# Performance work log

Measured on AMD Instinct MI355X. Metric: run time of the kernel, lower is better.

The kernel has to match this reference:

```python
import jax, jax.numpy as jnp
import numpy as np

# Search geometry (matches init_kwargs)
WS, WT, PS, K, STRIDE0 = 9, 1, 7, 10, 4
SEARCH_INPUT = "noisy"
ALPHA = 0.5
CRIT = "l2"


def _extract_patches(vid, ti, hi, wi):
    """vid: [T,H,W,C]; ti/hi/wi int32 with shape [...] (patch top-left corners).
    Returns [..., PS*PS*C] with clamped (edge-replicated) boundary handling."""
    T, H, W, C = vid.shape
    dy = jnp.arange(PS)
    dx = jnp.arange(PS)
    hh = jnp.clip(hi[..., None, None] + dy[:, None], 0, H - 1)  # [...,PS,1]
    ww = jnp.clip(wi[..., None, None] + dx[None, :], 0, W - 1)  # [...,1,PS]
    p = vid[ti[..., None, None], hh, ww]  # [...,PS,PS,C]
    return p.reshape(p.shape[:-3] + (PS * PS * C,))


def _nls(vid, fflow, bflow):
    """NonLocalSearch: vid [T,H,W,C], flows [T,H,W,2] (channel 0 = x/w, 1 = y/h).
    Returns (topk_dists [nq,K], inds = (ti,hi,wi,tk,hk,wk))."""
    T, H, W, C = vid.shape
    nH, nW = H // STRIDE0, W // STRIDE0
    ti, hi, wi = jnp.meshgrid(jnp.arange(T), jnp.arange(nH) * STRIDE0,
                              jnp.arange(nW) * STRIDE0, indexing="ij")
    ti, hi, wi = ti.reshape(-1), hi.reshape(-1), wi.reshape(-1)  # [nq]
    q = _extract_patches(vid, ti, hi, wi)  # [nq, PS*PS*C]

    ff = fflow[ti, hi, wi]  # [nq,2] flow to frame t+1
    bf = bflow[ti, hi, wi]  # [nq,2] flow to frame t-1
    zero = jnp.zeros_like(ff)
    flow_dt = jnp.stack([bf, zero, ff], axis=1)  # [nq, 2*WT+1, 2] for dt=-1,0,+1
    dts = jnp.arange(-WT, WT + 1)
    tj = jnp.clip(ti[:, None] + dts[None, :], 0, T - 1)  # [nq, 2*WT+1]
    bh = jnp.clip(hi[:, None] + jnp.round(flow_dt[..., 1]).astype(jnp.int32), 0, H - 1)
    bw = jnp.clip(wi[:, None] + jnp.round(flow_dt[..., 0]).astype(jnp.int32), 0, W - 1)

    # Candidate schedule: (dt_index, oy, ox) for all (2*WT+1)*WS*WS candidates.
    r = WS // 2
    oy, ox = np.meshgrid(np.arange(-r, r + 1), np.arange(-r, r + 1), indexing="ij")
    nt = 2 * WT + 1
    specs = np.stack([np.repeat(np.arange(nt), WS * WS),
                      np.tile(oy.ravel(), nt),
                      np.tile(ox.ravel(), nt)], axis=1).astype(np.int32)  # [S,3]

    def step(_, spec):
        di, sy, sx = spec[0], spec[1], spec[2]
        tjc = tj[:, di]
        hj = jnp.clip(bh[:, di] + sy, 0, H - 1)
        wj = jnp.clip(bw[:, di] + sx, 0, W - 1)
        cp = _extract_patches(vid, tjc, hj, wj)  # [nq,D]
        d = jnp.sum((q - cp) ** 2, axis=-1)  # L2 patch distance, [nq]
        return None, (d, tjc, hj, wj)

    _, (dists, tjs, hjs, wjs) = jax.lax.scan(step, None, jnp.asarray(specs))
    # dists: [S, nq] -> top-K smallest per query
    negd, idx = jax.lax.top_k(-dists.T, K)  # [nq,K]
    tk = jnp.take_along_axis(tjs.T, idx, axis=1)
    hk = jnp.take_along_axis(hjs.T, idx, axis=1)
    wk = jnp.take_along_axis(wjs.T, idx, axis=1)
    return -negd, (ti, hi, wi, tk, hk, wk)


def _refine(vid, inds):
    """RefineSearch with wr=1,kr=1: recompute L2 patch distances at given inds."""
    ti, hi, wi, tk, hk, wk = inds
    q = _extract_patches(vid, ti, hi, wi)          # [nq, D]
    cp = _extract_patches(vid, tk, hk, wk)         # [nq, K, D]
    return jnp.sum((q[:, None, :] - cp) ** 2, axis=-1)  # [nq, K]


def setup_inputs() -> dict:
    key = jax.random.key(0)
    k1, k2, k3, k4 = jax.random.split(key, 4)
    B, T, C, H, W = 1, 5, 3, 384, 384
    noisy = jax.random.normal(k1, (B, T, C, H, W), dtype=jnp.float32)
    deno = jax.random.normal(k2, (B, T, C, H, W), dtype=jnp.float32)
    fflow = jax.random.normal(k3, (B, T, 2, H, W), dtype=jnp.float32)
    bflow = jax.random.normal(k4, (B, T, 2, H, W), dtype=jnp.float32)
    return {"noisy": noisy, "deno": deno, "fflow": fflow, "bflow": bflow}


def reference(noisy, deno, fflow, bflow):
    def per_video(nv, dv, ff, bf):
        nv_t = jnp.transpose(nv, (0, 2, 3, 1))  # [T,H,W,C]
        dv_t = jnp.transpose(dv, (0, 2, 3, 1))
        ff_t = jnp.transpose(ff, (0, 2, 3, 1))  # [T,H,W,2]
        bf_t = jnp.transpose(bf, (0, 2, 3, 1))
        if SEARCH_INPUT == "noisy":
            srch = nv_t
        elif SEARCH_INPUT == "deno":
            srch = dv_t
        else:  # interp
            srch = ALPHA * nv_t + (1.0 - ALPHA) * dv_t
        _, inds = _nls(srch, ff_t, bf_t)
        return _refine(nv_t, inds)  # [nq, K]

    dists = jax.vmap(per_video)(noisy, deno, fflow, bflow)  # [B, nq, K]
    if CRIT == "l1":
        return jnp.mean(jnp.sqrt(dists))
    return jnp.mean(dists)
```

## Files before the change

### kernel.cpp

```cpp
#include <hip/hip_runtime.h>

#define TT 5
#define HH 384
#define WW 384
#define CC 3
#define WSR 4
#define NH_ 96
#define NW_ 96
#define NQ_ (TT*NH_*NW_)
#define NCAND 243
#define KK 10

#define RROW 12
#define RSST 13

typedef _Float16 h2v __attribute__((ext_vector_type(2)));
union U32H2 { unsigned u; h2v h; };

static __device__ __forceinline__ unsigned pack_f16(float a, float b) {
    U32H2 u;
    u.h.x = (_Float16)a; u.h.y = (_Float16)b;
    return u.u;
}

static __device__ __forceinline__ unsigned wave_min63(unsigned x) {
    x = min(x, (unsigned)__builtin_amdgcn_update_dpp((int)x,(int)x,0x121,0xF,0xF,false));
    x = min(x, (unsigned)__builtin_amdgcn_update_dpp((int)x,(int)x,0x122,0xF,0xF,false));
    x = min(x, (unsigned)__builtin_amdgcn_update_dpp((int)x,(int)x,0x124,0xF,0xF,false));
    x = min(x, (unsigned)__builtin_amdgcn_update_dpp((int)x,(int)x,0x128,0xF,0xF,false));
    x = min(x, (unsigned)__builtin_amdgcn_update_dpp((int)x,(int)x,0x142,0xF,0xF,false));
    x = min(x, (unsigned)__builtin_amdgcn_update_dpp((int)x,(int)x,0x143,0xF,0xF,false));
    return x;
}

__global__ __launch_bounds__(256) void nls_kernel(
    const float* __restrict__ vid,
    const float* __restrict__ fflow,
    const float* __restrict__ bflow,
    float* __restrict__ ws)
{
    const int q   = blockIdx.x;
    const int tid = threadIdx.x;
    const int t   = q / (NH_*NW_);
    const int rem = q % (NH_*NW_);
    const int hi  = (rem / NW_) * 4;
    const int wi  = (rem % NW_) * 4;

    __shared__ alignas(16) unsigned reg_lds[135*RROW];
    __shared__ alignas(16) unsigned qp_lds[84];
    __shared__ alignas(16) float    rssd[189*RSST];
    __shared__ float dist[256];

    const float ffx = fflow[((t*2+0)*HH + hi)*WW + wi];
    const float ffy = fflow[((t*2+1)*HH + hi)*WW + wi];
    const float bfx = bflow[((t*2+0)*HH + hi)*WW + wi];
    const float bfy = bflow[((t*2+1)*HH + hi)*WW + wi];

    const int tj0 = max(t-1, 0);
    const int tj2 = min(t+1, TT-1);
    const int bh0 = min(max(hi + (int)rintf(bfy), 0), HH-1);
    const int bw0 = min(max(wi + (int)rintf(bfx), 0), WW-1);
    const int bh2 = min(max(hi + (int)rintf(ffy), 0), HH-1);
    const int bw2 = min(max(wi + (int)rintf(ffx), 0), WW-1);
    const int rm0 = max(bh0-WSR,0), rm1 = max(hi-WSR,0), rm2 = max(bh2-WSR,0);
    const int cm0 = max(bw0-WSR,0), cm1 = max(wi-WSR,0), cm2 = max(bw2-WSR,0);
    const int ca0 = cm0 & ~1,       ca1 = cm1 & ~1,      ca2 = cm2 & ~1;

    for (int i = tid; i < 270; i += 256) {
        int row = i >> 1, h = i & 1;
        int di  = row / 45; int r45 = row - di*45;
        int c   = r45 / 15; int r   = r45 - c*15;
        int tjd = (di==0)?tj0:((di==1)?t  :tj2);
        int rm  = (di==0)?rm0:((di==1)?rm1:rm2);
        int ca  = (di==0)?ca0:((di==1)?ca1:ca2);
        int rr  = min(rm + r, HH-1);
        const float* vrow = vid + (size_t)((tjd*CC+c)*HH + rr)*WW;
        int c0 = ca + 8*h;
        float f0,f1,f2,f3,f4,f5,f6,f7;
        if (ca <= 368) {
            float2 p0 = *(const float2*)(vrow + c0);
            float2 p1 = *(const float2*)(vrow + c0 + 2);
            float2 p2 = *(const float2*)(vrow + c0 + 4);
            float2 p3 = *(const float2*)(vrow + c0 + 6);
            f0=p0.x; f1=p0.y; f2=p1.x; f3=p1.y; f4=p2.x; f5=p2.y; f6=p3.x; f7=p3.y;
        } else {
            f0=vrow[min(c0,  WW-1)]; f1=vrow[min(c0+1,WW-1)];
            f2=vrow[min(c0+2,WW-1)]; f3=vrow[min(c0+3,WW-1)];
            f4=vrow[min(c0+4,WW-1)]; f5=vrow[min(c0+5,WW-1)];
            f6=vrow[min(c0+6,WW-1)]; f7=vrow[min(c0+7,WW-1)];
        }
        uint4 w;
        w.x = pack_f16(f0,f1); w.y = pack_f16(f2,f3);
        w.z = pack_f16(f4,f5); w.w = pack_f16(f6,f7);
        *(uint4*)&reg_lds[row*RROW + 4*h] = w;
    }
    if (tid < 84) {
        int c  = tid / 28;
        int rr = tid - c*28;
        int dy = rr >> 2;
        int k  = rr & 3;
        int row = min(hi+dy, HH-1);
        const float* vrow = vid + (size_t)((t*CC + c)*HH + row)*WW;
        float v0 = vrow[min(wi + 2*k, WW-1)];
        float v1 = (k==3) ? 0.0f : vrow[min(wi + 2*k + 1, WW-1)];
        qp_lds[tid] = pack_f16(v0, v1);
    }
    __syncthreads();

    if (tid < 189) {
        int di   = tid / 63; int r63 = tid - di*63;
        int roff = r63 / 7;  int dy  = r63 - roff*7;
        int rr   = roff + dy;
        float rs[10];
        #pragma unroll
        for (int w = 0; w < 10; w++) rs[w] = 0.f;
        #pragma unroll
        for (int c = 0; c < 3; c++) {
            int base = ((di*3 + c)*15 + rr)*RROW;
            uint4 va0 = *(const uint4*)&reg_lds[base];
            uint4 va1 = *(const uint4*)&reg_lds[base + 4];
            uint4 vq  = *(const uint4*)&qp_lds[c*28 + dy*4];
            unsigned A[8], B[8];
            A[0]=va0.x; A[1]=va0.y; A[2]=va0.z; A[3]=va0.w;
            A[4]=va1.x; A[5]=va1.y; A[6]=va1.z; A[7]=va1.w;
            #pragma unroll
            for (int j = 0; j < 7; j++) B[j] = (A[j] >> 16) | (A[j+1] << 16);
            B[7] = A[7] >> 16;
            U32H2 q0,q1,q2,q3;
            q0.u = vq.x; q1.u = vq.y; q2.u = vq.z; q3.u = vq.w;
            #pragma unroll
            for (int w = 0; w < 10; w++) {
                const int off = w >> 1;
                U32H2 c0,c1,c2,c3;
                if (w & 1) { c0.u=B[off]; c1.u=B[off+1]; c2.u=B[off+2]; c3.u=B[off+3]; }
                else       { c0.u=A[off]; c1.u=A[off+1]; c2.u=A[off+2]; c3.u=A[off+3]; }
                U32H2 d0,d1,d2,d3;
                d0.h = c0.h - q0.h;
                d1.h = c1.h - q1.h;
                d2.h = c2.h - q2.h;
                d3.h = c3.h - q3.h;
                d3.u &= 0x0000FFFFu;
                float s = rs[w];
                s = __builtin_amdgcn_fdot2(d0.h, d0.h, s, false);
                s = __builtin_amdgcn_fdot2(d1.h, d1.h, s, false);
                s = __builtin_amdgcn_fdot2(d2.h, d2.h, s, false);
                s = __builtin_amdgcn_fdot2(d3.h, d3.h, s, false);
                rs[w] = s;
            }
        }
        int ob = tid * RSST;
        #pragma unroll
        for (int w = 0; w < 10; w++) rssd[ob + w] = rs[w];
    }
    __syncthreads();

    float dmy = __int_as_float(0x7f800000);
    if (tid < NCAND) {
        int di  = tid / 81; int s81 = tid - di*81;
        int syq = s81 / 9;  int sx  = s81 - syq*9 - WSR;
        int sy  = syq - WSR;
        int bhd = (di==0)?bh0:((di==1)?hi :bh2);
        int bwd = (di==0)?bw0:((di==1)?wi :bw2);
        int rm  = (di==0)?rm0:((di==1)?rm1:rm2);
        int ca  = (di==0)?ca0:((di==1)?ca1:ca2);
        int hj = min(max(bhd + sy, 0), HH-1);
        int wj = min(max(bwd + sx, 0), WW-1);
        int roff = hj - rm;
        int wof  = wj - ca;
        int ib = (di*63 + roff*7)*RSST + wof;
        float s = 0.f;
        #pragma unroll
        for (int dy = 0; dy < 7; dy++) s += rssd[ib + dy*RSST];
        dmy = s;
    }
    dist[tid] = dmy;
    __syncthreads();

    if (tid < 64) {
        float v0 = dist[tid], v1 = dist[tid+64], v2 = dist[tid+128], v3 = dist[tid+192];
        unsigned k0 = (__float_as_uint(v0) & 0xFFFFFF00u) | (unsigned)tid;
        unsigned k1 = (__float_as_uint(v1) & 0xFFFFFF00u) | (unsigned)(tid+64);
        unsigned k2 = (__float_as_uint(v2) & 0xFFFFFF00u) | (unsigned)(tid+128);
        unsigned k3 = (__float_as_uint(v3) & 0xFFFFFF00u) | (unsigned)(tid+192);
        float sumk = 0.f;
        #pragma unroll 1
        for (int k = 0; k < KK; k++) {
            unsigned loc = min(min(k0,k1), min(k2,k3));
            unsigned wm  = wave_min63(loc);
            unsigned m   = (unsigned)__builtin_amdgcn_readlane((int)wm, 63);
            int slot = (int)(m & 0xFFu);
            int lw = slot & 63, jw = slot >> 6;
            int r0 = __builtin_amdgcn_readlane(__float_as_int(v0), lw);
            int r1 = __builtin_amdgcn_readlane(__float_as_int(v1), lw);
            int r2 = __builtin_amdgcn_readlane(__float_as_int(v2), lw);
            int r3 = __builtin_amdgcn_readlane(__float_as_int(v3), lw);
            int rv = (jw==0)?r0:((jw==1)?r1:((jw==2)?r2:r3));
            sumk += __int_as_float(rv);
            k0 = (slot == (int)tid      ) ? 0xFFFFFFFFu : k0;
            k1 = (slot == (int)tid + 64 ) ? 0xFFFFFFFFu : k1;
            k2 = (slot == (int)tid + 128) ? 0xFFFFFFFFu : k2;
            k3 = (slot == (int)tid + 192) ? 0xFFFFFFFFu : k3;
        }
        if (tid == 0) ws[q] = sumk;
    }
}

__global__ __launch_bounds__(256) void reduce1_kernel(
    const float* __restrict__ ws, float* __restrict__ out)
{
    float s = ws[blockIdx.x*256 + threadIdx.x];
    #pragma unroll
    for (int o = 32; o > 0; o >>= 1) s += __shfl_down(s, o, 64);
    __shared__ float sd[4];
    int w = threadIdx.x >> 6, l = threadIdx.x & 63;
    if (l == 0) sd[w] = s;
    __syncthreads();
    if (threadIdx.x == 0) {
        float tot = sd[0] + sd[1] + sd[2] + sd[3];
        atomicAdd(out, tot * (1.0f / ((float)NQ_ * (float)KK)));
    }
}

extern "C" void kernel_launch(void* const* d_in, const int* in_sizes, int n_in,
                              void* d_out, int out_size, void* d_ws, size_t ws_size,
                              hipStream_t stream) {
    const float* noisy = (const float*)d_in[0];
    const float* fflow = (const float*)d_in[2];
    const float* bflow = (const float*)d_in[3];
    float* ws  = (float*)d_ws;
    float* out = (float*)d_out;

    hipMemsetAsync(out, 0, sizeof(float), stream);
    nls_kernel<<<NQ_, 256, 0, stream>>>(noisy, fflow, bflow, ws);
    reduce1_kernel<<<NQ_/256, 256, 0, stream>>>(ws, out);
}
```

Baseline: 275.6 us.

## Fuse final reduction via atomics, remap blocks across XCDs, sum masked keys

Removes the second reduce kernel by having each query block atomically add its scaled top-k sum to the output. Remaps block indices so that neighbouring queries are grouped per XCD for cache locality. Replaces per-iteration readlane recovery of exact distances with the masked sort key, which slightly truncates the mantissa. This adds heavy atomic contention on one address and a small precision loss.

```diff
diff --git a/kernel.cpp b/kernel.cpp
--- a/kernel.cpp
+++ b/kernel.cpp
@@ -37,9 +37,10 @@
     const float* __restrict__ vid,
     const float* __restrict__ fflow,
     const float* __restrict__ bflow,
-    float* __restrict__ ws)
+    float* __restrict__ out)
 {
-    const int q   = blockIdx.x;
+    const int bid = blockIdx.x;
+    const int q   = (bid & 7) * (NQ_/8) + (bid >> 3);
     const int tid = threadIdx.x;
     const int t   = q / (NH_*NW_);
     const int rem = q % (NH_*NW_);
@@ -177,47 +178,25 @@
     __syncthreads();
 
     if (tid < 64) {
-        float v0 = dist[tid], v1 = dist[tid+64], v2 = dist[tid+128], v3 = dist[tid+192];
-        unsigned k0 = (__float_as_uint(v0) & 0xFFFFFF00u) | (unsigned)tid;
-        unsigned k1 = (__float_as_uint(v1) & 0xFFFFFF00u) | (unsigned)(tid+64);
-        unsigned k2 = (__float_as_uint(v2) & 0xFFFFFF00u) | (unsigned)(tid+128);
-        unsigned k3 = (__float_as_uint(v3) & 0xFFFFFF00u) | (unsigned)(tid+192);
+        unsigned k0 = (__float_as_uint(dist[tid    ]) & 0xFFFFFF00u) | (unsigned)tid;
+        unsigned k1 = (__float_as_uint(dist[tid+ 64]) & 0xFFFFFF00u) | (unsigned)(tid+64);
+        unsigned k2 = (__float_as_uint(dist[tid+128]) & 0xFFFFFF00u) | (unsigned)(tid+128);
+        unsigned k3 = (__float_as_uint(dist[tid+192]) & 0xFFFFFF00u) | (unsigned)(tid+192);
         float sumk = 0.f;
         #pragma unroll 1
         for (int k = 0; k < KK; k++) {
             unsigned loc = min(min(k0,k1), min(k2,k3));
             unsigned wm  = wave_min63(loc);
             unsigned m   = (unsigned)__builtin_amdgcn_readlane((int)wm, 63);
+            sumk += __uint_as_float(m & 0xFFFFFF00u);
             int slot = (int)(m & 0xFFu);
-            int lw = slot & 63, jw = slot >> 6;
-            int r0 = __builtin_amdgcn_readlane(__float_as_int(v0), lw);
-            int r1 = __builtin_amdgcn_readlane(__float_as_int(v1), lw);
-            int r2 = __builtin_amdgcn_readlane(__float_as_int(v2), lw);
-            int r3 = __builtin_amdgcn_readlane(__float_as_int(v3), lw);
-            int rv = (jw==0)?r0:((jw==1)?r1:((jw==2)?r2:r3));
-            sumk += __int_as_float(rv);
             k0 = (slot == (int)tid      ) ? 0xFFFFFFFFu : k0;
             k1 = (slot == (int)tid + 64 ) ? 0xFFFFFFFFu : k1;
             k2 = (slot == (int)tid + 128) ? 0xFFFFFFFFu : k2;
             k3 = (slot == (int)tid + 192) ? 0xFFFFFFFFu : k3;
         }
-        if (tid == 0) ws[q] = sumk;
-    }
-}
-
-__global__ __launch_bounds__(256) void reduce1_kernel(
-    const float* __restrict__ ws, float* __restrict__ out)
-{
-    float s = ws[blockIdx.x*256 + threadIdx.x];
-    #pragma unroll
-    for (int o = 32; o > 0; o >>= 1) s += __shfl_down(s, o, 64);
-    __shared__ float sd[4];
-    int w = threadIdx.x >> 6, l = threadIdx.x & 63;
-    if (l == 0) sd[w] = s;
-    __syncthreads();
-    if (threadIdx.x == 0) {
-        float tot = sd[0] + sd[1] + sd[2] + sd[3];
-        atomicAdd(out, tot * (1.0f / ((float)NQ_ * (float)KK)));
+        if (tid == 0)
+            atomicAdd(out, sumk * (1.0f / ((float)NQ_ * (float)KK)));
     }
 }
 
@@ -227,10 +206,8 @@
     const float* noisy = (const float*)d_in[0];
     const float* fflow = (const float*)d_in[2];
     const float* bflow = (const float*)d_in[3];
-    float* ws  = (float*)d_ws;
     float* out = (float*)d_out;
 
     hipMemsetAsync(out, 0, sizeof(float), stream);
-    nls_kernel<<<NQ_, 256, 0, stream>>>(noisy, fflow, bflow, ws);
-    reduce1_kernel<<<NQ_/256, 256, 0, stream>>>(ws, out);
-}
+    nls_kernel<<<NQ_, 256, 0, stream>>>(noisy, fflow, bflow, out);
+}
```

Result: slower. 670.1 us (+143.2%).
